# Kernel tuning notes

Hardware: AMD Instinct MI355X
Metric: run time of the kernel (lower is better)

## Reference

```python
import jax, jax.numpy as jnp
import numpy as np

N, E, L, D, H, NC = 50000, 400000, 1024, 256, 4, 2
C = D // H  # per-head dim


def setup_inputs() -> dict:
    key = jax.random.key(0)
    ks = jax.random.split(key, 12)
    s = 1.0 / np.sqrt(L)
    sd = 1.0 / np.sqrt(D)
    return {
        "x": jax.random.normal(ks[0], (N, L), dtype=jnp.float32),
        "edge_index": jax.random.randint(ks[1], (2, E), 0, N, dtype=jnp.int32),
        "label": 1,
        "Wq": jax.random.normal(ks[2], (L, D), dtype=jnp.float32) * s,
        "bq": jnp.zeros((D,), dtype=jnp.float32),
        "Wk": jax.random.normal(ks[3], (L, D), dtype=jnp.float32) * s,
        "bk": jnp.zeros((D,), dtype=jnp.float32),
        "Wv": jax.random.normal(ks[4], (L, D), dtype=jnp.float32) * s,
        "bv": jnp.zeros((D,), dtype=jnp.float32),
        "Wskip": jax.random.normal(ks[5], (L, D), dtype=jnp.float32) * s,
        "bskip": jnp.zeros((D,), dtype=jnp.float32),
        "gate_w": jax.random.normal(ks[6], (D, NC), dtype=jnp.float32) * sd,
        "gate_b": jnp.zeros((NC,), dtype=jnp.float32),
        "pool_w": jax.random.normal(ks[7], (D, D), dtype=jnp.float32) * sd,
        "pool_b": jnp.zeros((D,), dtype=jnp.float32),
    }


def reference(x, edge_index, label, Wq, bq, Wk, bk, Wv, bv, Wskip, bskip,
              gate_w, gate_b, pool_w, pool_b):
    src, dst = edge_index[0], edge_index[1]
    # per-head projections [N, H, C]
    q = (x @ Wq + bq).reshape(N, H, C)
    k = (x @ Wk + bk).reshape(N, H, C)
    v = (x @ Wv + bv).reshape(N, H, C)
    # edge attention scores, softmax over incoming edges per destination node
    s = jnp.einsum('ehc,ehc->eh', q[dst], k[src]) / np.sqrt(C)  # [E, H]
    m = jax.ops.segment_max(s, dst, num_segments=N)             # [N, H]
    ex = jnp.exp(s - m[dst])
    den = jax.ops.segment_sum(ex, dst, num_segments=N)          # [N, H]
    alpha = ex / den[dst]                                       # [E, H]
    agg = jax.ops.segment_sum(alpha[:, :, None] * v[src], dst,
                              num_segments=N).reshape(N, D)
    h = agg + x @ Wskip + bskip                                 # root/skip term
    h = jax.nn.gelu(h, approximate=False)
    # global adaptive attention pooling: per-class softmax over nodes
    scores = h @ gate_w + gate_b                                # [N, NC]
    attn = jax.nn.softmax(scores, axis=0)                       # [N, NC]
    y = jnp.einsum('nc,nd->cd', attn, h @ pool_w + pool_b)      # [NC, D]
    A = attn[:, label]
    return (y, attn, h, A)
```

## Files before the change

### kernel.cpp

```cpp
#include <hip/hip_runtime.h>
#include <stdint.h>

#define N_NODES 50000
#define N_EDGES 400000
#define M_PAD   50048

typedef __attribute__((ext_vector_type(8))) __bf16 bf16x8;
typedef __attribute__((ext_vector_type(4))) float floatx4;

__device__ __forceinline__ unsigned short f2bf(float f) {
    unsigned int u = __float_as_uint(f);
    unsigned int r = (u + 0x7fffu + ((u >> 16) & 1u)) >> 16;
    return (unsigned short)r;
}

__device__ __forceinline__ float bf2f(unsigned short u) {
    return __uint_as_float(((unsigned int)u) << 16);
}

__device__ __forceinline__ void gload_lds16(const void* g, void* l) {
    __builtin_amdgcn_global_load_lds((__attribute__((address_space(1))) void*)g,
                                     (__attribute__((address_space(3))) void*)l,
                                     16, 0, 0);
}

__global__ void k_pre(const float* __restrict__ x, unsigned short* __restrict__ xb,
                      const float* __restrict__ Wq, const float* __restrict__ Wk,
                      const float* __restrict__ Wv, const float* __restrict__ Ws,
                      const float* __restrict__ bq, const float* __restrict__ bk,
                      const float* __restrict__ bv, const float* __restrict__ bs,
                      unsigned short* __restrict__ WT, float* __restrict__ biascat,
                      const int* __restrict__ ei, int* __restrict__ cnt) {
    int bid = blockIdx.x;
    if (bid < 4096) {
        const int total = M_PAD * 256;
        for (int u = bid * 256 + threadIdx.x; u < total; u += 4096 * 256) {
            int row = u >> 8;
            int c4  = u & 255;
            float4 v = make_float4(0.f, 0.f, 0.f, 0.f);
            if (row < N_NODES) v = ((const float4*)x)[(size_t)row * 256 + c4];
            ushort4 o;
            o.x = f2bf(v.x); o.y = f2bf(v.y); o.z = f2bf(v.z); o.w = f2bf(v.w);
            ((ushort4*)xb)[u] = o;
        }
    } else if (bid < 8192) {
        int idx = (bid - 4096) * 256 + threadIdx.x;
        int n = idx >> 10;
        int k = idx & 1023;
        int g = n >> 8, d = n & 255;
        const float* W = (g == 0) ? Wq : (g == 1) ? Wk : (g == 2) ? Wv : Ws;
        WT[idx] = f2bf(W[k * 256 + d]);
        if (idx < 1024) {
            int g2 = idx >> 8, d2 = idx & 255;
            const float* B = (g2 == 0) ? bq : (g2 == 1) ? bk : (g2 == 2) ? bv : bs;
            biascat[idx] = B[d2];
        }
    } else {
        int e = (bid - 8192) * 256 + threadIdx.x;
        if (e < N_EDGES) atomicAdd(&cnt[ei[N_EDGES + e]], 1);
    }
}

__global__ void k_scan(const int* __restrict__ cnt, int* __restrict__ offs) {
    __shared__ int wsums[4];
    const int CH = 196;
    int t = threadIdx.x;
    int beg = t * CH;
    int end = beg + CH; if (end > N_NODES) end = N_NODES;
    int s = 0;
    for (int i = beg; i < end; i++) s += cnt[i];
    int lane = t & 63, w = t >> 6;
    int v = s;
#pragma unroll
    for (int off = 1; off < 64; off <<= 1) {
        int u = __shfl_up(v, off, 64);
        if (lane >= off) v += u;
    }
    if (lane == 63) wsums[w] = v;
    __syncthreads();
    int carry = 0;
    for (int i = 0; i < w; i++) carry += wsums[i];
    int run = carry + v - s;
    for (int i = beg; i < end; i++) {
        offs[i] = run;
        run += cnt[i];
    }
    if (t == 255) offs[N_NODES] = run;
}

__launch_bounds__(256)
__global__ void k_gemm(const unsigned short* __restrict__ A,
                       const unsigned short* __restrict__ BT,
                       const float* __restrict__ bias,
                       float* __restrict__ qbuf, unsigned short* __restrict__ kvb,
                       float* __restrict__ sbuf,
                       const int* __restrict__ ei, const int* __restrict__ offs,
                       int* __restrict__ fill, int* __restrict__ ssrc) {
    __shared__ unsigned short As[128 * 32];
    __shared__ unsigned short Bs[128 * 32];

    int wg = blockIdx.x;
    if (wg >= 3136) {
        int e = (wg - 3136) * 256 + threadIdx.x;
        if (e < N_EDGES) {
            int src = ei[e];
            int dst = ei[N_EDGES + e];
            int pos = offs[dst] + atomicAdd(&fill[dst], 1);
            ssrc[pos] = src;
        }
        return;
    }

    int xcd  = wg & 7;
    int j    = wg >> 3;
    int xt   = j & 7;
    int ygrp = j >> 3;
    int yt   = ygrp * 8 + xcd;
    if (yt >= 391) return;

    const int row0 = yt * 128;
    const int col0 = xt * 128;

    const int t = threadIdx.x;
    const int w = t >> 6;
    const int l = t & 63;

    const int lr = l >> 2;
    const int lc = (l & 3) * 8;

    const int wr = (w >> 1) * 64;
    const int wc = (w & 1) * 64;
    const int lane15 = l & 15;
    const int quad = l >> 4;

    floatx4 acc[4][4];
#pragma unroll
    for (int i = 0; i < 4; i++)
#pragma unroll
        for (int j2 = 0; j2 < 4; j2++) acc[i][j2] = (floatx4)0.f;

    for (int kk = 0; kk < 1024; kk += 32) {
        __syncthreads();
#pragma unroll
        for (int issue = 0; issue < 2; issue++) {
            int arow = row0 + issue * 64 + w * 16 + lr;
            gload_lds16(A + (size_t)arow * 1024 + kk + lc, As + issue * 2048 + w * 512);
            int brow = col0 + issue * 64 + w * 16 + lr;
            gload_lds16(BT + (size_t)brow * 1024 + kk + lc, Bs + issue * 2048 + w * 512);
        }
        __builtin_amdgcn_s_waitcnt(0x0f70);
        __syncthreads();

        bf16x8 af[4], bfr[4];
#pragma unroll
        for (int i = 0; i < 4; i++) {
            af[i]  = *(const bf16x8*)(As + (wr + i * 16 + lane15) * 32 + quad * 8);
            bfr[i] = *(const bf16x8*)(Bs + (wc + i * 16 + lane15) * 32 + quad * 8);
        }
#pragma unroll
        for (int i = 0; i < 4; i++)
#pragma unroll
            for (int j2 = 0; j2 < 4; j2++)
                acc[i][j2] = __builtin_amdgcn_mfma_f32_16x16x32_bf16(af[i], bfr[j2], acc[i][j2], 0, 0, 0);
    }

#pragma unroll
    for (int i = 0; i < 4; i++) {
#pragma unroll
        for (int j2 = 0; j2 < 4; j2++) {
            int col = col0 + wc + j2 * 16 + lane15;
            int g = col >> 8;
            int d = col & 255;
            float bcol = bias[col];
#pragma unroll
            for (int r = 0; r < 4; r++) {
                int row = row0 + wr + i * 16 + quad * 4 + r;
                float val = acc[i][j2][r] + bcol;
                if (g == 0)      qbuf[(size_t)row * 256 + d] = val;
                else if (g == 1) kvb[(size_t)row * 512 + d] = f2bf(val);
                else if (g == 2) kvb[(size_t)row * 512 + 256 + d] = f2bf(val);
                else             sbuf[(size_t)row * 256 + d] = val;
            }
        }
    }
}

__launch_bounds__(256)
__global__ void k_attn(const int* __restrict__ offs, const int* __restrict__ ssrc,
                       const float* __restrict__ qbuf, const unsigned short* __restrict__ kvb,
                       const float* __restrict__ sbuf,
                       const float* __restrict__ gate_w, const float* __restrict__ gate_b,
                       float* __restrict__ out_h, float* __restrict__ exsc) {
    __shared__ float4 lacc[4][64];
    __shared__ float  lden[4][64];
    int w = threadIdx.x >> 6, l = threadIdx.x & 63;
    int n = blockIdx.x;

    float4 qv = ((const float4*)(qbuf + (size_t)n * 256))[l];
    int beg = offs[n], end = offs[n + 1];

    float4 acc = make_float4(0.f, 0.f, 0.f, 0.f);
    float den = 0.f;

    for (int base = beg; base < end; base += 256) {
        int m = end - base; if (m > 256) m = 256;
        int eIdx = w + 4 * l;
        int mysrc = (eIdx < m) ? ssrc[base + eIdx] : 0;
        int nIter = (m > w) ? ((m - w + 3) >> 2) : 0;
        for (int jj = 0; jj < nIter; jj++) {
            int src = __shfl(mysrc, jj, 64);
            const unsigned short* row = kvb + (size_t)src * 512;
            ushort4 ku = ((const ushort4*)row)[l];
            ushort4 vu = ((const ushort4*)(row + 256))[l];
            float p = qv.x * bf2f(ku.x) + qv.y * bf2f(ku.y) +
                      qv.z * bf2f(ku.z) + qv.w * bf2f(ku.w);
            p += __shfl_xor(p, 1, 16);
            p += __shfl_xor(p, 2, 16);
            p += __shfl_xor(p, 4, 16);
            p += __shfl_xor(p, 8, 16);
            float ex = expf(p * 0.125f);
            den += ex;
            acc.x += ex * bf2f(vu.x); acc.y += ex * bf2f(vu.y);
            acc.z += ex * bf2f(vu.z); acc.w += ex * bf2f(vu.w);
        }
    }

    lacc[w][l] = acc;
    lden[w][l] = den;
    __syncthreads();
    if (w != 0) return;

    float4 a0 = lacc[0][l], a1 = lacc[1][l], a2 = lacc[2][l], a3 = lacc[3][l];
    acc.x = a0.x + a1.x + a2.x + a3.x;
    acc.y = a0.y + a1.y + a2.y + a3.y;
    acc.z = a0.z + a1.z + a2.z + a3.z;
    acc.w = a0.w + a1.w + a2.w + a3.w;
    den = lden[0][l] + lden[1][l] + lden[2][l] + lden[3][l];

    float inv = (den > 0.f) ? 1.f / den : 0.f;
    float4 sk = ((const float4*)(sbuf + (size_t)n * 256))[l];

    float z0 = acc.x * inv + sk.x;
    float z1 = acc.y * inv + sk.y;
    float z2 = acc.z * inv + sk.z;
    float z3 = acc.w * inv + sk.w;

    const float is2 = 0.70710678118f;
    float h0 = 0.5f * z0 * (1.f + erff(z0 * is2));
    float h1 = 0.5f * z1 * (1.f + erff(z1 * is2));
    float h2 = 0.5f * z2 * (1.f + erff(z2 * is2));
    float h3 = 0.5f * z3 * (1.f + erff(z3 * is2));
    ((float4*)(out_h + (size_t)n * 256))[l] = make_float4(h0, h1, h2, h3);

    int d0 = l * 4;
    float s0 = h0 * gate_w[(d0 + 0) * 2] + h1 * gate_w[(d0 + 1) * 2] +
               h2 * gate_w[(d0 + 2) * 2] + h3 * gate_w[(d0 + 3) * 2];
    float s1 = h0 * gate_w[(d0 + 0) * 2 + 1] + h1 * gate_w[(d0 + 1) * 2 + 1] +
               h2 * gate_w[(d0 + 2) * 2 + 1] + h3 * gate_w[(d0 + 3) * 2 + 1];
#pragma unroll
    for (int off = 1; off < 64; off <<= 1) {
        s0 += __shfl_xor(s0, off, 64);
        s1 += __shfl_xor(s1, off, 64);
    }
    if (l == 0) {
        exsc[n * 2 + 0] = expf(s0 + gate_b[0]);
        exsc[n * 2 + 1] = expf(s1 + gate_b[1]);
    }
}

__global__ void k_esum(const float* __restrict__ exsc, float* __restrict__ esum) {
    __shared__ float red0[4], red1[4];
    float p0 = 0.f, p1 = 0.f;
    for (int n = blockIdx.x * blockDim.x + threadIdx.x; n < N_NODES; n += gridDim.x * blockDim.x) {
        p0 += exsc[n * 2];
        p1 += exsc[n * 2 + 1];
    }
#pragma unroll
    for (int off = 1; off < 64; off <<= 1) {
        p0 += __shfl_xor(p0, off, 64);
        p1 += __shfl_xor(p1, off, 64);
    }
    int w = threadIdx.x >> 6, l = threadIdx.x & 63;
    if (l == 0) { red0[w] = p0; red1[w] = p1; }
    __syncthreads();
    if (threadIdx.x == 0) {
        atomicAdd(&esum[0], red0[0] + red0[1] + red0[2] + red0[3]);
        atomicAdd(&esum[1], red1[0] + red1[1] + red1[2] + red1[3]);
    }
}

__global__ void k_t(const float* __restrict__ exsc, const float* __restrict__ esum,
                    const float* __restrict__ h_f, const int* __restrict__ label_p,
                    float* __restrict__ attn_out, float* __restrict__ A_out,
                    float* __restrict__ t_ws) {
    int d = threadIdx.x;
    float inv0 = 1.f / esum[0], inv1 = 1.f / esum[1];
    int lab = *label_p;
    int n0 = blockIdx.x * 98;
    int n1 = n0 + 98; if (n1 > N_NODES) n1 = N_NODES;
    float t0 = 0.f, t1 = 0.f;
    for (int n = n0; n < n1; n++) {
        float e0 = exsc[n * 2], e1 = exsc[n * 2 + 1];
        float a0 = e0 * inv0, a1 = e1 * inv1;
        float hv = h_f[(size_t)n * 256 + d];
        t0 += a0 * hv;
        t1 += a1 * hv;
        if (d == 0) attn_out[n * 2] = a0;
        else if (d == 1) attn_out[n * 2 + 1] = a1;
        else if (d == 2) A_out[n] = (lab == 0) ? a0 : a1;
    }
    atomicAdd(&t_ws[d], t0);
    atomicAdd(&t_ws[256 + d], t1);
}

__global__ void k_y(const float* __restrict__ t_ws, const float* __restrict__ pool_w,
                    const float* __restrict__ pool_b, float* __restrict__ y_out) {
    int d = threadIdx.x;
    float a0 = pool_b[d], a1 = pool_b[d];
    for (int k = 0; k < 256; k++) {
        float w = pool_w[k * 256 + d];
        a0 += t_ws[k] * w;
        a1 += t_ws[256 + k] * w;
    }
    y_out[d] = a0;
    y_out[256 + d] = a1;
}

extern "C" void kernel_launch(void* const* d_in, const int* in_sizes, int n_in,
                              void* d_out, int out_size, void* d_ws, size_t ws_size,
                              hipStream_t stream) {
    const float* x      = (const float*)d_in[0];
    const int*   ei     = (const int*)d_in[1];
    const int*   label  = (const int*)d_in[2];
    const float* Wq     = (const float*)d_in[3];
    const float* bq     = (const float*)d_in[4];
    const float* Wk     = (const float*)d_in[5];
    const float* bk     = (const float*)d_in[6];
    const float* Wv     = (const float*)d_in[7];
    const float* bv     = (const float*)d_in[8];
    const float* Wskip  = (const float*)d_in[9];
    const float* bskip  = (const float*)d_in[10];
    const float* gate_w = (const float*)d_in[11];
    const float* gate_b = (const float*)d_in[12];
    const float* pool_w = (const float*)d_in[13];
    const float* pool_b = (const float*)d_in[14];

    char* ws = (char*)d_ws;
    size_t off = 0;
    float* qbuf = (float*)(ws + off);                 off += (size_t)M_PAD * 256 * 4;
    unsigned short* kvb = (unsigned short*)(ws + off);off += (size_t)M_PAD * 512 * 2;
    float* sbuf = (float*)(ws + off);                 off += (size_t)M_PAD * 256 * 4;
    unsigned short* xb = (unsigned short*)(ws + off); off += (size_t)M_PAD * 1024 * 2;
    unsigned short* WT = (unsigned short*)(ws + off); off += (size_t)1024 * 1024 * 2;
    float* biascat = (float*)(ws + off);              off += 1024 * 4;
    int* cnt  = (int*)(ws + off);                     off += (size_t)N_NODES * 4;
    int* fill = (int*)(ws + off);                     off += (size_t)N_NODES * 4;
    int* offs = (int*)(ws + off);                     off += (size_t)(N_NODES + 1) * 4;
    int* ssrc = (int*)(ws + off);                     off += (size_t)N_EDGES * 4;
    float* exsc = (float*)(ws + off);                 off += (size_t)N_NODES * 2 * 4;
    float* esum = (float*)(ws + off);                 off += 2 * 4;
    float* t_ws = (float*)(ws + off);                 off += 512 * 4;

    float* out = (float*)d_out;
    float* y_out    = out;
    float* attn_out = out + 512;
    float* h_out    = out + 100512;
    float* A_out    = out + 12900512;

    hipMemsetAsync(cnt, 0, (size_t)N_NODES * 2 * 4, stream);
    hipMemsetAsync(esum, 0, (2 + 512) * 4, stream);

    k_pre<<<9755, 256, 0, stream>>>(x, xb, Wq, Wk, Wv, Wskip, bq, bk, bv, bskip,
                                    WT, biascat, ei, cnt);
    k_scan<<<1, 256, 0, stream>>>(cnt, offs);
    k_gemm<<<4699, 256, 0, stream>>>(xb, WT, biascat, qbuf, kvb, sbuf,
                                     ei, offs, fill, ssrc);
    k_attn<<<N_NODES, 256, 0, stream>>>(offs, ssrc, qbuf, kvb, sbuf, gate_w, gate_b,
                                        h_out, exsc);
    k_esum<<<128, 256, 0, stream>>>(exsc, esum);
    k_t<<<512, 256, 0, stream>>>(exsc, esum, h_out, label, attn_out, A_out, t_ws);
    k_y<<<1, 256, 0, stream>>>(t_ws, pool_w, pool_b, y_out);
}
```

Baseline: 755.2 us.

## Double-buffer GEMM LDS tiles and XOR-swizzle to avoid bank conflicts

Splits the projection GEMM's LDS staging into two buffers so the next K-tile's global-to-LDS loads are in flight while the current tile feeds the MFMAs. It also XOR-swizzles the 16-byte chunk column on both write and read to reduce LDS bank conflicts on fragment loads. The cost is twice the LDS per block, which may lower occupancy, plus extra barriers and more complex waitcnt handling.

After: 796.2 us. 5.4% more time.

```diff
diff --git a/kernel.cpp b/kernel.cpp
--- a/kernel.cpp
+++ b/kernel.cpp
@@ -96,8 +96,8 @@
                        float* __restrict__ sbuf,
                        const int* __restrict__ ei, const int* __restrict__ offs,
                        int* __restrict__ fill, int* __restrict__ ssrc) {
-    __shared__ unsigned short As[128 * 32];
-    __shared__ unsigned short Bs[128 * 32];
+    __shared__ unsigned short As[2 * 4096];
+    __shared__ unsigned short Bs[2 * 4096];
 
     int wg = blockIdx.x;
     if (wg >= 3136) {
@@ -126,12 +126,13 @@
     const int l = t & 63;
 
     const int lr = l >> 2;
-    const int lc = (l & 3) * 8;
+    const int lcg = ((l & 3) ^ ((l >> 3) & 3)) * 8;
 
     const int wr = (w >> 1) * 64;
     const int wc = (w & 1) * 64;
     const int lane15 = l & 15;
     const int quad = l >> 4;
+    const int qx = quad ^ ((lane15 >> 1) & 3);
 
     floatx4 acc[4][4];
 #pragma unroll
@@ -139,30 +140,65 @@
 #pragma unroll
         for (int j2 = 0; j2 < 4; j2++) acc[i][j2] = (floatx4)0.f;
 
-    for (int kk = 0; kk < 1024; kk += 32) {
+#define STAGE(buf, ktn)                                                                   \
+    {                                                                                     \
+        const int kko = (ktn) * 32;                                                       \
+        _Pragma("unroll")                                                                 \
+        for (int issue = 0; issue < 2; issue++) {                                         \
+            int arow = row0 + issue * 64 + w * 16 + lr;                                   \
+            gload_lds16(A + (size_t)arow * 1024 + kko + lcg,                              \
+                        As + (buf) * 4096 + issue * 2048 + w * 512);                      \
+            int brow = col0 + issue * 64 + w * 16 + lr;                                   \
+            gload_lds16(BT + (size_t)brow * 1024 + kko + lcg,                             \
+                        Bs + (buf) * 4096 + issue * 2048 + w * 512);                      \
+        }                                                                                 \
+    }
+
+#define COMPUTE(buf)                                                                      \
+    {                                                                                     \
+        const unsigned short* Ab = As + (buf) * 4096;                                     \
+        const unsigned short* Bb = Bs + (buf) * 4096;                                     \
+        bf16x8 af[4], bfr[4];                                                             \
+        _Pragma("unroll")                                                                 \
+        for (int i = 0; i < 4; i++) {                                                     \
+            af[i]  = *(const bf16x8*)(Ab + (wr + i * 16 + lane15) * 32 + qx * 8);         \
+            bfr[i] = *(const bf16x8*)(Bb + (wc + i * 16 + lane15) * 32 + qx * 8);         \
+        }                                                                                 \
+        _Pragma("unroll")                                                                 \
+        for (int i = 0; i < 4; i++)                                                       \
+            _Pragma("unroll")                                                             \
+            for (int j2 = 0; j2 < 4; j2++)                                                \
+                acc[i][j2] = __builtin_amdgcn_mfma_f32_16x16x32_bf16(af[i], bfr[j2],      \
+                                                                    acc[i][j2], 0, 0, 0);\
+    }
+
+    STAGE(0, 0);
+    STAGE(1, 1);
+    __builtin_amdgcn_s_waitcnt(0x0f74);
+    __syncthreads();
+
+    for (int kt = 0; kt < 32; kt += 2) {
+        COMPUTE(0);
         __syncthreads();
-#pragma unroll
-        for (int issue = 0; issue < 2; issue++) {
-            int arow = row0 + issue * 64 + w * 16 + lr;
-            gload_lds16(A + (size_t)arow * 1024 + kk + lc, As + issue * 2048 + w * 512);
-            int brow = col0 + issue * 64 + w * 16 + lr;
-            gload_lds16(BT + (size_t)brow * 1024 + kk + lc, Bs + issue * 2048 + w * 512);
-        }
-        __builtin_amdgcn_s_waitcnt(0x0f70);
+        if (kt + 2 < 32) {
+            STAGE(0, kt + 2);
+            __builtin_amdgcn_s_waitcnt(0x0f74);
+        } else {
+            __builtin_amdgcn_s_waitcnt(0x0f70);
+        }
         __syncthreads();
 
-        bf16x8 af[4], bfr[4];
-#pragma unroll
-        for (int i = 0; i < 4; i++) {
-            af[i]  = *(const bf16x8*)(As + (wr + i * 16 + lane15) * 32 + quad * 8);
-            bfr[i] = *(const bf16x8*)(Bs + (wc + i * 16 + lane15) * 32 + quad * 8);
-        }
-#pragma unroll
-        for (int i = 0; i < 4; i++)
-#pragma unroll
-            for (int j2 = 0; j2 < 4; j2++)
-                acc[i][j2] = __builtin_amdgcn_mfma_f32_16x16x32_bf16(af[i], bfr[j2], acc[i][j2], 0, 0, 0);
-    }
+        COMPUTE(1);
+        if (kt + 1 < 31) {
+            __syncthreads();
+            STAGE(1, kt + 3);
+            __builtin_amdgcn_s_waitcnt(0x0f74);
+            __syncthreads();
+        }
+    }
+
+#undef STAGE
+#undef COMPUTE
 
 #pragma unroll
     for (int i = 0; i < 4; i++) {
```
